# Kernel tuning notes

Hardware: AMD Instinct MI355X
Metric: run time of the kernel (lower is better)

The kernel has to match this reference:

```python
import jax, jax.numpy as jnp
import numpy as np

N_NODES = 50000
N_EDGES = 400000
D = 300          # num_features == hidden_units
L = 5            # num_layers
C = 128          # num_outputs
NG = 256         # graphs per batch
BN_EPS = 1e-5


def setup_inputs() -> dict:
    key = jax.random.key(0)
    ks = jax.random.split(key, 16)
    x = jax.random.normal(ks[0], (N_NODES, D), dtype=jnp.float32)
    edge_index = jax.random.randint(ks[1], (2, N_EDGES), 0, N_NODES, dtype=jnp.int64)
    batch = jnp.sort(jax.random.randint(ks[2], (N_NODES,), 0, NG, dtype=jnp.int64))
    s = 1.0 / np.sqrt(D)
    # Stacked per-layer GINConv MLP params: Linear -> BN -> ReLU -> Linear, then outer BN
    mlp_W1 = jax.random.uniform(ks[3], (L, D, D), jnp.float32, -s, s)
    mlp_b1 = jax.random.uniform(ks[4], (L, D), jnp.float32, -s, s)
    mlp_g1 = jnp.ones((L, D), jnp.float32)
    mlp_be1 = jnp.zeros((L, D), jnp.float32)
    mlp_W2 = jax.random.uniform(ks[5], (L, D, D), jnp.float32, -s, s)
    mlp_b2 = jax.random.uniform(ks[6], (L, D), jnp.float32, -s, s)
    bn_g = jnp.ones((L, D), jnp.float32)
    bn_b = jnp.zeros((L, D), jnp.float32)
    # num_layers+1 readout heads (num_features == hidden_units so all [D, C])
    fc_W = jax.random.uniform(ks[7], (L + 1, D, C), jnp.float32, -s, s)
    fc_b = jax.random.uniform(ks[8], (L + 1, C), jnp.float32, -s, s)
    return dict(x=x, edge_index=edge_index, batch=batch,
                mlp_W1=mlp_W1, mlp_b1=mlp_b1, mlp_g1=mlp_g1, mlp_be1=mlp_be1,
                mlp_W2=mlp_W2, mlp_b2=mlp_b2, bn_g=bn_g, bn_b=bn_b,
                fc_W=fc_W, fc_b=fc_b)


def _bn(h, gamma, beta):
    # BatchNorm1d in training mode: biased batch stats over the node dim
    mu = h.mean(axis=0)
    var = h.var(axis=0)
    return (h - mu) * jax.lax.rsqrt(var + BN_EPS) * gamma + beta


def reference(x, edge_index, batch, mlp_W1, mlp_b1, mlp_g1, mlp_be1,
              mlp_W2, mlp_b2, bn_g, bn_b, fc_W, fc_b):
    src, dst = edge_index[0], edge_index[1]
    n = x.shape[0]
    outs = [x]
    h = x
    for i in range(L):
        # GINConv (eps=0): MLP(x + sum_{j in N(i)} x_j), scatter-add over edges
        agg = jax.ops.segment_sum(h[src], dst, num_segments=n)
        z = h + agg
        z = z @ mlp_W1[i] + mlp_b1[i]
        z = jax.nn.relu(_bn(z, mlp_g1[i], mlp_be1[i]))
        z = z @ mlp_W2[i] + mlp_b2[i]
        h = jax.nn.relu(_bn(z, bn_g[i], bn_b[i]))  # outer BN + ReLU
        outs.append(h)
    # global mean pool per graph, then per-depth linear heads summed (dropout off in eval)
    counts = jax.ops.segment_sum(jnp.ones((n,), x.dtype), batch, num_segments=NG)
    inv = 1.0 / jnp.maximum(counts, 1.0)
    out = jnp.zeros((NG, C), x.dtype)
    for i, hi in enumerate(outs):
        pooled = jax.ops.segment_sum(hi, batch, num_segments=NG) * inv[:, None]
        out = out + (pooled @ fc_W[i] + fc_b[i])
    return out
```

## Files before the change

kernel.cpp:

```cpp
#include <hip/hip_runtime.h>

#define D 300
#define KP 320
#define NPAD 50048
#define NT128 391
#define NTPAD 392
#define PSL 3136
#define PSLIVE 3128
#define WSTRIDE 328
#define NGR 256
#define NL 5
#define NC 128
#define BN_EPS 1e-5f

typedef __attribute__((ext_vector_type(8))) short bf16x8;
typedef __attribute__((ext_vector_type(4))) float f32x4;
typedef unsigned short u16;

__device__ __forceinline__ void atomAdd(float* p, float v) { unsafeAtomicAdd(p, v); }

__device__ __forceinline__ short f2bf(float f) {
    union { float f; unsigned u; } v; v.f = f;
    unsigned r = v.u + 0x7fffu + ((v.u >> 16) & 1u);
    return (short)(r >> 16);
}
__device__ __forceinline__ float bf2f(short s) {
    union { unsigned u; float f; } v;
    v.u = ((unsigned)(u16)s) << 16;
    return v.f;
}
__device__ __forceinline__ unsigned cvtpk(float lo, float hi) {
    unsigned r;
    asm("v_cvt_pk_bf16_f32 %0, %1, %2" : "=v"(r) : "v"(lo), "v"(hi));
    return r;
}
template<int C>
__device__ __forceinline__ float rs_add(float v) {
    int x = __builtin_amdgcn_update_dpp(0, __float_as_int(v), C, 0xF, 0xF, true);
    return v + __int_as_float(x);
}
__device__ __forceinline__ float red16(float v) {
    v = rs_add<0x111>(v);
    v = rs_add<0x112>(v);
    v = rs_add<0x114>(v);
    v = rs_add<0x118>(v);
    return v;
}

__global__ void offsets_kernel(const int* __restrict__ batch, int* __restrict__ off, int N) {
    int g = threadIdx.x;
    if (g > NGR) return;
    int lo = 0, hi = N;
    while (lo < hi) {
        int mid = (lo + hi) >> 1;
        if (batch[mid] < g) lo = mid + 1; else hi = mid;
    }
    off[g] = lo;
}

__global__ __launch_bounds__(256)
void deg_kernel(const int* __restrict__ ei, int* __restrict__ deg, int E) {
    int e = blockIdx.x * 256 + threadIdx.x;
    if (e < E) atomicAdd(&deg[ei[E + e]], 1);
}

__global__ __launch_bounds__(256)
void degpart_kernel(const int* __restrict__ deg, int* __restrict__ part, int N) {
    int i = blockIdx.x * 256 + threadIdx.x;
    int v = (i < N) ? deg[i] : 0;
    #pragma unroll
    for (int o = 1; o < 64; o <<= 1) v += __shfl_xor(v, o);
    __shared__ int ws[4];
    if ((threadIdx.x & 63) == 0) ws[threadIdx.x >> 6] = v;
    __syncthreads();
    if (threadIdx.x == 0) part[blockIdx.x] = ws[0] + ws[1] + ws[2] + ws[3];
}

__global__ __launch_bounds__(256)
void partscan_kernel(int* __restrict__ part, int nb) {
    __shared__ int buf[256];
    int t = threadIdx.x;
    int v = (t < nb) ? part[t] : 0;
    buf[t] = v;
    __syncthreads();
    for (int o = 1; o < 256; o <<= 1) {
        int u = (t >= o) ? buf[t - o] : 0;
        __syncthreads();
        buf[t] += u;
        __syncthreads();
    }
    if (t < nb) part[t] = (t == 0) ? 0 : buf[t - 1];
}

__global__ __launch_bounds__(256)
void rowptr_kernel(const int* __restrict__ deg, const int* __restrict__ part,
                   int* __restrict__ rowptr, int N, int E) {
    __shared__ int buf[256];
    int b = blockIdx.x, t = threadIdx.x;
    int i = b * 256 + t;
    int v = (i < N) ? deg[i] : 0;
    buf[t] = v;
    __syncthreads();
    for (int o = 1; o < 256; o <<= 1) {
        int u = (t >= o) ? buf[t - o] : 0;
        __syncthreads();
        buf[t] += u;
        __syncthreads();
    }
    if (i < N) rowptr[i] = part[b] + buf[t] - v;
    if (b == 0 && t == 0) rowptr[N] = E;
}

__global__ __launch_bounds__(256)
void fill_kernel(const int* __restrict__ ei, const int* __restrict__ rowptr,
                 int* __restrict__ cursor, int* __restrict__ col, int E) {
    int e = blockIdx.x * 256 + threadIdx.x;
    if (e >= E) return;
    int src = ei[e];
    int dst = ei[E + e];
    int pos = atomicAdd(&cursor[dst], 1);
    col[rowptr[dst] + pos] = src;
}

__global__ __launch_bounds__(256)
void wcvt_kernel(const float* __restrict__ W1, const float* __restrict__ W2,
                 u16* __restrict__ Wt) {
    int idx = blockIdx.x * 256 + threadIdx.x;
    if (idx >= 10 * KP * 80) return;
    int n4 = idx % 80;
    int k = (idx / 80) % KP;
    int mat = idx / (80 * KP);
    const float* Wsrc = (mat < NL) ? (W1 + (size_t)mat * D * D) : (W2 + (size_t)(mat - NL) * D * D);
    float4 w = make_float4(0.f, 0.f, 0.f, 0.f);
    if (k < D && n4 < 75) w = *(const float4*)(Wsrc + (size_t)k * D + n4 * 4);
    size_t base = ((size_t)mat * 320 + n4 * 4) * KP + k;
    Wt[base]          = (u16)f2bf(w.x);
    Wt[base + KP]     = (u16)f2bf(w.y);
    Wt[base + 2 * KP] = (u16)f2bf(w.z);
    Wt[base + 3 * KP] = (u16)f2bf(w.w);
}

__global__ __launch_bounds__(256)
void xcvt_kernel(const float* __restrict__ x, u16* __restrict__ xbf, int N) {
    int idx = blockIdx.x * 256 + threadIdx.x;
    if (idx >= NPAD * 40) return;
    int row = idx / 40;
    int c8 = (idx - row * 40) * 8;
    short o[8];
    #pragma unroll
    for (int i = 0; i < 8; ++i) {
        int c = c8 + i;
        float f = (row < N && c < D) ? x[(size_t)row * D + c] : 0.f;
        o[i] = f2bf(f);
    }
    *(bf16x8*)(xbf + (size_t)row * KP + c8) = *(bf16x8*)o;
}

template<bool APPLY>
__global__ __launch_bounds__(256)
void gather_kernel(const u16* __restrict__ H, u16* __restrict__ Z,
                   const int* __restrict__ rowptr, const int* __restrict__ col,
                   const float* __restrict__ scsh, int N) {
    int idx = blockIdx.x * 256 + threadIdx.x;
    if (idx >= N * 40) return;
    int node = idx / 40;
    int c8 = (idx - node * 40) * 8;
    float sc[8], sh[8];
    if (APPLY) {
        #pragma unroll
        for (int i = 0; i < 8; ++i) { sc[i] = scsh[c8 + i]; sh[i] = scsh[KP + c8 + i]; }
    }
    int s = rowptr[node], e = rowptr[node + 1];
    bf16x8 v = *(const bf16x8*)(H + (size_t)node * KP + c8);
    float acc[8];
    #pragma unroll
    for (int i = 0; i < 8; ++i) {
        float f = bf2f(v[i]);
        acc[i] = APPLY ? fmaxf(fmaf(f, sc[i], sh[i]), 0.f) : f;
    }
    int j = s;
    for (; j + 4 <= e; j += 4) {
        int s0 = col[j], s1 = col[j + 1], s2 = col[j + 2], s3 = col[j + 3];
        bf16x8 w0 = *(const bf16x8*)(H + (size_t)s0 * KP + c8);
        bf16x8 w1 = *(const bf16x8*)(H + (size_t)s1 * KP + c8);
        bf16x8 w2 = *(const bf16x8*)(H + (size_t)s2 * KP + c8);
        bf16x8 w3 = *(const bf16x8*)(H + (size_t)s3 * KP + c8);
        #pragma unroll
        for (int i = 0; i < 8; ++i) {
            float f0 = bf2f(w0[i]);
            float f1 = bf2f(w1[i]);
            float f2 = bf2f(w2[i]);
            float f3 = bf2f(w3[i]);
            acc[i] += APPLY ? fmaxf(fmaf(f0, sc[i], sh[i]), 0.f) : f0;
            acc[i] += APPLY ? fmaxf(fmaf(f1, sc[i], sh[i]), 0.f) : f1;
            acc[i] += APPLY ? fmaxf(fmaf(f2, sc[i], sh[i]), 0.f) : f2;
            acc[i] += APPLY ? fmaxf(fmaf(f3, sc[i], sh[i]), 0.f) : f3;
        }
    }
    for (; j < e; ++j) {
        int s0 = col[j];
        bf16x8 w0 = *(const bf16x8*)(H + (size_t)s0 * KP + c8);
        #pragma unroll
        for (int i = 0; i < 8; ++i) {
            float f0 = bf2f(w0[i]);
            acc[i] += APPLY ? fmaxf(fmaf(f0, sc[i], sh[i]), 0.f) : f0;
        }
    }
    short o[8];
    #pragma unroll
    for (int i = 0; i < 8; ++i) o[i] = f2bf(acc[i]);
    *(bf16x8*)(Z + (size_t)node * KP + c8) = *(bf16x8*)o;
}

template<bool APPLY>
__global__ __launch_bounds__(320)
void pool_kernel(const u16* __restrict__ H, const int* __restrict__ off,
                 const float* __restrict__ scsh, float* __restrict__ pooled_l) {
    __shared__ float red[8][KP];
    int t = threadIdx.x;
    int g = blockIdx.x;
    int rq = t / 40;
    int c8 = (t - rq * 40) * 8;
    float sc[8], sh[8];
    if (APPLY) {
        #pragma unroll
        for (int i = 0; i < 8; ++i) { sc[i] = scsh[c8 + i]; sh[i] = scsh[KP + c8 + i]; }
    }
    int r0 = off[g], r1 = off[g + 1];
    float a[8] = {};
    for (int r = r0 + rq; r < r1; r += 8) {
        bf16x8 v = *(const bf16x8*)(H + (size_t)r * KP + c8);
        #pragma unroll
        for (int i = 0; i < 8; ++i) {
            float f = bf2f(v[i]);
            a[i] += APPLY ? fmaxf(fmaf(f, sc[i], sh[i]), 0.f) : f;
        }
    }
    #pragma unroll
    for (int i = 0; i < 8; ++i) red[rq][c8 + i] = a[i];
    __syncthreads();
    int c = t;
    if (c < D) {
        float s = 0.f;
        #pragma unroll
        for (int j = 0; j < 8; ++j) s += red[j][c];
        pooled_l[g * D + c] = s;
    }
}

template<bool APPLY>
__global__ __launch_bounds__(512, 6)
void mfma_gemm_kernel(const u16* __restrict__ Abf, const u16* __restrict__ Wt,
                      const float* __restrict__ scsh,
                      u16* __restrict__ Cbf, float* __restrict__ psum, int Nreal) {
    __shared__ u16 Ws[80 * WSTRIDE];
    const int tid = threadIdx.x;
    const int bid = blockIdx.x;
    const int xcd = bid & 7;
    const int pos = bid >> 3;
    const int tile = xcd + ((pos >> 2) << 3);
    const int nBase = (pos & 3) * 80;
    if (tile >= NT128) return;
    const int wave = tid >> 6, lane = tid & 63;
    const int quad = lane >> 4, l16 = lane & 15;

    const u16* pA = Abf + (size_t)(tile * 128 + wave * 16 + l16) * KP + quad * 8;
    bf16x8 a[10];
    #pragma unroll
    for (int kc = 0; kc < 10; ++kc) a[kc] = *(const bf16x8*)(pA + kc * 32);

    {
        const u16* src = Wt + (size_t)nBase * KP;
        for (int unit = tid; unit < 80 * 40; unit += 512) {
            int n = unit / 40, kg = unit - n * 40;
            int kc = kg >> 2, q = kg & 3;
            *(bf16x8*)&Ws[n * WSTRIDE + kc * 32 + ((q ^ (n & 3)) << 3)] =
                *(const bf16x8*)(src + (size_t)n * KP + kg * 8);
        }
    }

    #pragma unroll
    for (int kc = 0; kc < 10; ++kc) asm volatile("" : "+v"(a[kc]));
    __syncthreads();

    if (APPLY) {
        #pragma unroll
        for (int kc = 0; kc < 10; ++kc) {
            const float* sp = scsh + kc * 32 + quad * 8;
            float4 s0 = *(const float4*)sp;
            float4 s1 = *(const float4*)(sp + 4);
            float4 h0 = *(const float4*)(sp + KP);
            float4 h1 = *(const float4*)(sp + KP + 4);
            float sc[8] = {s0.x, s0.y, s0.z, s0.w, s1.x, s1.y, s1.z, s1.w};
            float sh[8] = {h0.x, h0.y, h0.z, h0.w, h1.x, h1.y, h1.z, h1.w};
            float f[8];
            #pragma unroll
            for (int i = 0; i < 8; ++i)
                f[i] = fmaxf(fmaf(bf2f(a[kc][i]), sc[i], sh[i]), 0.f);
            union { unsigned u[4]; bf16x8 v; } o;
            o.u[0] = cvtpk(f[0], f[1]);
            o.u[1] = cvtpk(f[2], f[3]);
            o.u[2] = cvtpk(f[4], f[5]);
            o.u[3] = cvtpk(f[6], f[7]);
            a[kc] = o.v;
        }
    }

    int wb[5];
    #pragma unroll
    for (int nt = 0; nt < 5; ++nt)
        wb[nt] = (nt * 16 + l16) * WSTRIDE + ((quad ^ (l16 & 3)) << 3);

    f32x4 acc[5] = {};
    __builtin_amdgcn_s_setprio(1);
    #pragma unroll
    for (int kc = 0; kc < 10; ++kc) {
        #pragma unroll
        for (int nt = 0; nt < 5; ++nt) {
            bf16x8 b = *(const bf16x8*)&Ws[wb[nt] + kc * 32];
            acc[nt] = __builtin_amdgcn_mfma_f32_16x16x32_bf16(b, a[kc], acc[nt], 0, 0, 0);
        }
    }
    __builtin_amdgcn_s_setprio(0);

    const int r0g = tile * 128 + wave * 16 + l16;
    const bool ok = r0g < Nreal;
    u16* crow = Cbf + (size_t)r0g * KP + nBase + quad * 4;
    const int pslot = tile * 8 + wave;
    float* psq = psum + (size_t)320 * PSL;
    #pragma unroll
    for (int nt = 0; nt < 5; ++nt) {
        float v0 = acc[nt][0], v1 = acc[nt][1], v2 = acc[nt][2], v3 = acc[nt][3];
        uint2 w;
        w.x = cvtpk(v0, v1);
        w.y = cvtpk(v2, v3);
        *(uint2*)(crow + nt * 16) = w;
        float m0 = ok ? v0 : 0.f, m1 = ok ? v1 : 0.f;
        float m2 = ok ? v2 : 0.f, m3 = ok ? v3 : 0.f;
        float sv0 = red16(m0), qv0 = red16(m0 * m0);
        float sv1 = red16(m1), qv1 = red16(m1 * m1);
        float sv2 = red16(m2), qv2 = red16(m2 * m2);
        float sv3 = red16(m3), qv3 = red16(m3 * m3);
        if (l16 == 15) {
            int c = nBase + nt * 16 + quad * 4;
            psum[(size_t)(c + 0) * PSL + pslot] = sv0;
            psum[(size_t)(c + 1) * PSL + pslot] = sv1;
            psum[(size_t)(c + 2) * PSL + pslot] = sv2;
            psum[(size_t)(c + 3) * PSL + pslot] = sv3;
            psq [(size_t)(c + 0) * PSL + pslot] = qv0;
            psq [(size_t)(c + 1) * PSL + pslot] = qv1;
            psq [(size_t)(c + 2) * PSL + pslot] = qv2;
            psq [(size_t)(c + 3) * PSL + pslot] = qv3;
        }
    }
}

__global__ __launch_bounds__(256)
void bnfin_kernel(const float* __restrict__ psum, const float* __restrict__ g,
                  const float* __restrict__ be, float* __restrict__ scsh, float invN) {
    int c = blockIdx.x;
    const float* ps = psum + (size_t)c * PSL;
    const float* pq = psum + (size_t)(320 + c) * PSL;
    float s1 = 0.f, s2 = 0.f;
    for (int i = threadIdx.x; i < PSLIVE; i += 256) { s1 += ps[i]; s2 += pq[i]; }
    #pragma unroll
    for (int o = 1; o < 64; o <<= 1) { s1 += __shfl_xor(s1, o); s2 += __shfl_xor(s2, o); }
    __shared__ float w1[4], w2[4];
    int wv = threadIdx.x >> 6;
    if ((threadIdx.x & 63) == 0) { w1[wv] = s1; w2[wv] = s2; }
    __syncthreads();
    if (threadIdx.x == 0) {
        float t1 = w1[0] + w1[1] + w1[2] + w1[3];
        float t2 = w2[0] + w2[1] + w2[2] + w2[3];
        float mu = t1 * invN;
        float var = t2 * invN - mu * mu;
        float s = g[c] / sqrtf(var + BN_EPS);
        scsh[c] = s;
        scsh[KP + c] = fmaf(-mu, s, be[c]);
    }
}

__global__ __launch_bounds__(128)
void bias_init_kernel(const float* __restrict__ fcb, float* __restrict__ out) {
    int i = blockIdx.x * 128 + threadIdx.x;
    if (i >= NGR * NC) return;
    int c = i & (NC - 1);
    float s = 0.f;
    for (int l = 0; l <= NL; ++l) s += fcb[l * NC + c];
    out[i] = s;
}

__global__ __launch_bounds__(128)
void readout_kernel(const float* __restrict__ pooled, const int* __restrict__ off,
                    const float* __restrict__ fcW, float* __restrict__ out) {
    __shared__ float sp[4][D];
    int c = threadIdx.x;
    int l = blockIdx.y;
    int g0 = blockIdx.x * 4;
    for (int i = c; i < 4 * D; i += 128) {
        int gg = i / D, k = i - gg * D;
        sp[gg][k] = pooled[((size_t)l * NGR + g0 + gg) * D + k];
    }
    __syncthreads();
    float acc[4] = {0.f, 0.f, 0.f, 0.f};
    for (int k = 0; k < D; ++k) {
        float w = fcW[((size_t)l * D + k) * NC + c];
        #pragma unroll
        for (int gg = 0; gg < 4; ++gg) acc[gg] = fmaf(sp[gg][k], w, acc[gg]);
    }
    #pragma unroll
    for (int gg = 0; gg < 4; ++gg) {
        int g = g0 + gg;
        float inv = 1.0f / fmaxf((float)(off[g + 1] - off[g]), 1.0f);
        atomAdd(&out[g * NC + c], acc[gg] * inv);
    }
}

extern "C" void kernel_launch(void* const* d_in, const int* in_sizes, int n_in,
                              void* d_out, int out_size, void* d_ws, size_t ws_size,
                              hipStream_t stream) {
    const float* x       = (const float*)d_in[0];
    const int*   ei      = (const int*)d_in[1];
    const int*   batch   = (const int*)d_in[2];
    const float* W1  = (const float*)d_in[3];
    const float* g1  = (const float*)d_in[5];
    const float* be1 = (const float*)d_in[6];
    const float* W2  = (const float*)d_in[7];
    const float* bng = (const float*)d_in[9];
    const float* bnb = (const float*)d_in[10];
    const float* fcW = (const float*)d_in[11];
    const float* fcb = (const float*)d_in[12];
    float* out = (float*)d_out;

    const int N = in_sizes[0] / D;
    const int E = in_sizes[1] / 2;
    const int nb = (N + 255) / 256;

    u16* xbf  = (u16*)d_ws;
    float* psum = (float*)d_ws;
    u16* bufA = xbf + (size_t)NPAD * KP;
    u16* bufB = bufA + (size_t)NPAD * KP;
    u16* Wt   = bufB + (size_t)NPAD * KP;
    float* pooled = (float*)(Wt + (size_t)10 * 320 * KP);
    float* sc1    = pooled + (size_t)(NL + 1) * NGR * D;
    float* sc2    = sc1 + 2 * KP;
    int*   off    = (int*)(sc2 + 2 * KP);
    int*   rowptr = off + NGR + 1;
    int*   cursor = rowptr + N + 1;
    int*   col    = cursor + N;
    int*   part   = col + E;

    hipMemsetAsync(sc1, 0, 4 * KP * sizeof(float), stream);
    offsets_kernel<<<1, 320, 0, stream>>>(batch, off, N);
    bias_init_kernel<<<(NGR * NC + 127) / 128, 128, 0, stream>>>(fcb, out);

    hipMemsetAsync(cursor, 0, N * sizeof(int), stream);
    deg_kernel<<<(E + 255) / 256, 256, 0, stream>>>(ei, cursor, E);
    degpart_kernel<<<nb, 256, 0, stream>>>(cursor, part, N);
    partscan_kernel<<<1, 256, 0, stream>>>(part, nb);
    rowptr_kernel<<<nb, 256, 0, stream>>>(cursor, part, rowptr, N, E);
    hipMemsetAsync(cursor, 0, N * sizeof(int), stream);
    fill_kernel<<<(E + 255) / 256, 256, 0, stream>>>(ei, rowptr, cursor, col, E);

    wcvt_kernel<<<(10 * KP * 80 + 255) / 256, 256, 0, stream>>>(W1, W2, Wt);
    xcvt_kernel<<<(NPAD * 40 + 255) / 256, 256, 0, stream>>>(x, xbf, N);

    const int gemm_blocks = 8 * 49 * 4;
    const int nd40 = N * 40;
    float invN = 1.0f / (float)N;
    const size_t WtM = (size_t)320 * KP;

    pool_kernel<false><<<NGR, 320, 0, stream>>>(xbf, off, sc2, pooled);

    u16* g = bufA;
    u16* t = bufB;
    const u16* src = xbf;
    for (int l = 0; l < NL; ++l) {
        if (l == 0)
            gather_kernel<false><<<(nd40 + 255) / 256, 256, 0, stream>>>(src, g, rowptr, col, sc2, N);
        else
            gather_kernel<true><<<(nd40 + 255) / 256, 256, 0, stream>>>(src, g, rowptr, col, sc2, N);
        mfma_gemm_kernel<false><<<gemm_blocks, 512, 0, stream>>>(
            g, Wt + (size_t)l * WtM, sc1, t, psum, N);
        bnfin_kernel<<<D, 256, 0, stream>>>(psum, g1 + l * D, be1 + l * D, sc1, invN);
        mfma_gemm_kernel<true><<<gemm_blocks, 512, 0, stream>>>(
            t, Wt + (size_t)(NL + l) * WtM, sc1, g, psum, N);
        bnfin_kernel<<<D, 256, 0, stream>>>(psum, bng + l * D, bnb + l * D, sc2, invN);
        pool_kernel<true><<<NGR, 320, 0, stream>>>(g, off, sc2, pooled + (size_t)(l + 1) * NGR * D);
        src = g;
        u16* tmp = g; g = t; t = tmp;
    }
    readout_kernel<<<dim3(NGR / 4, NL + 1), 128, 0, stream>>>(pooled, off, fcW, out);
}
```

Measured before the change: 1.058 ms.

## Swap GEMM operand roles: weights in registers, activation tile via direct LDS loads

The MFMA GEMM now keeps each wave's 16-column slice of the weight matrix in registers and stages the 128-row activation tile into LDS using global_load_lds direct copies. Each of 5 waves covers all 8 row groups, and the fused BN+ReLU apply runs in place on the LDS tile. Per-tile BN partial sums are accumulated across row groups before the cross-lane reduction, which shrinks the partial-sum buffer from per-wave to per-tile slots. The block grows to 80KB of LDS with 320 threads and a lower occupancy hint. This trades occupancy for fewer redundant weight loads and less reduction work.

```diff
diff --git a/kernel.cpp b/kernel.cpp
--- a/kernel.cpp
+++ b/kernel.cpp
@@ -4,10 +4,8 @@
 #define KP 320
 #define NPAD 50048
 #define NT128 391
-#define NTPAD 392
-#define PSL 3136
-#define PSLIVE 3128
-#define WSTRIDE 328
+#define PSL 392
+#define PSLIVE 391
 #define NGR 256
 #define NL 5
 #define NC 128
@@ -45,6 +43,10 @@
     v = rs_add<0x114>(v);
     v = rs_add<0x118>(v);
     return v;
+}
+__device__ __forceinline__ void gload_lds16(const u16* g, u16* l) {
+    __builtin_amdgcn_global_load_lds((const __attribute__((address_space(1))) void*)g,
+                                     (__attribute__((address_space(3))) void*)l, 16, 0, 0);
 }
 
 __global__ void offsets_kernel(const int* __restrict__ batch, int* __restrict__ off, int N) {
@@ -249,11 +251,11 @@
 }
 
 template<bool APPLY>
-__global__ __launch_bounds__(512, 6)
+__global__ __launch_bounds__(320, 2)
 void mfma_gemm_kernel(const u16* __restrict__ Abf, const u16* __restrict__ Wt,
                       const float* __restrict__ scsh,
                       u16* __restrict__ Cbf, float* __restrict__ psum, int Nreal) {
-    __shared__ u16 Ws[80 * WSTRIDE];
+    __shared__ u16 Ab[40960];
     const int tid = threadIdx.x;
     const int bid = blockIdx.x;
     const int xcd = bid & 7;
@@ -261,96 +263,102 @@
     const int tile = xcd + ((pos >> 2) << 3);
     const int nBase = (pos & 3) * 80;
     if (tile >= NT128) return;
-    const int wave = tid >> 6, lane = tid & 63;
+    const int wave = tid >> 6;
+    const int lane = tid & 63;
     const int quad = lane >> 4, l16 = lane & 15;
 
-    const u16* pA = Abf + (size_t)(tile * 128 + wave * 16 + l16) * KP + quad * 8;
-    bf16x8 a[10];
-    #pragma unroll
-    for (int kc = 0; kc < 10; ++kc) a[kc] = *(const bf16x8*)(pA + kc * 32);
-
+    bf16x8 bw[10];
     {
-        const u16* src = Wt + (size_t)nBase * KP;
-        for (int unit = tid; unit < 80 * 40; unit += 512) {
-            int n = unit / 40, kg = unit - n * 40;
-            int kc = kg >> 2, q = kg & 3;
-            *(bf16x8*)&Ws[n * WSTRIDE + kc * 32 + ((q ^ (n & 3)) << 3)] =
-                *(const bf16x8*)(src + (size_t)n * KP + kg * 8);
-        }
-    }
-
-    #pragma unroll
-    for (int kc = 0; kc < 10; ++kc) asm volatile("" : "+v"(a[kc]));
+        const u16* wp = Wt + (size_t)(nBase + wave * 16 + l16) * KP + quad * 8;
+        #pragma unroll
+        for (int kc = 0; kc < 10; ++kc) bw[kc] = *(const bf16x8*)(wp + kc * 32);
+    }
+
+    {
+        const u16* base = Abf + (size_t)tile * 128 * KP;
+        #pragma unroll
+        for (int i = 0; i < 16; ++i) {
+            int c = i * 320 + tid;
+            int t6 = c >> 6;
+            int rg = (t6 * 205) >> 11;
+            int kc = t6 - rg * 10;
+            int go = (rg * 16 + l16) * KP + kc * 32 + quad * 8;
+            gload_lds16(base + go, &Ab[c * 8]);
+        }
+    }
     __syncthreads();
 
     if (APPLY) {
-        #pragma unroll
-        for (int kc = 0; kc < 10; ++kc) {
-            const float* sp = scsh + kc * 32 + quad * 8;
-            float4 s0 = *(const float4*)sp;
-            float4 s1 = *(const float4*)(sp + 4);
-            float4 h0 = *(const float4*)(sp + KP);
-            float4 h1 = *(const float4*)(sp + KP + 4);
-            float sc[8] = {s0.x, s0.y, s0.z, s0.w, s1.x, s1.y, s1.z, s1.w};
-            float sh[8] = {h0.x, h0.y, h0.z, h0.w, h1.x, h1.y, h1.z, h1.w};
+        float sca[2][8], sha[2][8];
+        #pragma unroll
+        for (int h = 0; h < 2; ++h) {
+            int k0 = (2 * wave + h) * 32 + quad * 8;
+            float4 s0 = *(const float4*)(scsh + k0);
+            float4 s1 = *(const float4*)(scsh + k0 + 4);
+            float4 h0 = *(const float4*)(scsh + KP + k0);
+            float4 h1 = *(const float4*)(scsh + KP + k0 + 4);
+            sca[h][0]=s0.x; sca[h][1]=s0.y; sca[h][2]=s0.z; sca[h][3]=s0.w;
+            sca[h][4]=s1.x; sca[h][5]=s1.y; sca[h][6]=s1.z; sca[h][7]=s1.w;
+            sha[h][0]=h0.x; sha[h][1]=h0.y; sha[h][2]=h0.z; sha[h][3]=h0.w;
+            sha[h][4]=h1.x; sha[h][5]=h1.y; sha[h][6]=h1.z; sha[h][7]=h1.w;
+        }
+        #pragma unroll
+        for (int j = 0; j < 16; ++j) {
+            const int h = j & 1, rg = j >> 1;
+            u16* p = &Ab[((rg * 10 + 2 * wave + h) << 9) + lane * 8];
+            bf16x8 v = *(const bf16x8*)p;
             float f[8];
             #pragma unroll
             for (int i = 0; i < 8; ++i)
-                f[i] = fmaxf(fmaf(bf2f(a[kc][i]), sc[i], sh[i]), 0.f);
+                f[i] = fmaxf(fmaf(bf2f(v[i]), sca[h][i], sha[h][i]), 0.f);
             union { unsigned u[4]; bf16x8 v; } o;
             o.u[0] = cvtpk(f[0], f[1]);
             o.u[1] = cvtpk(f[2], f[3]);
             o.u[2] = cvtpk(f[4], f[5]);
             o.u[3] = cvtpk(f[6], f[7]);
-            a[kc] = o.v;
-        }
-    }
-
-    int wb[5];
-    #pragma unroll
-    for (int nt = 0; nt < 5; ++nt)
-        wb[nt] = (nt * 16 + l16) * WSTRIDE + ((quad ^ (l16 & 3)) << 3);
-
-    f32x4 acc[5] = {};
+            *(bf16x8*)p = o.v;
+        }
+        __syncthreads();
+    }
+
+    const int lbase = lane * 8;
+    f32x4 acc[8] = {};
     __builtin_amdgcn_s_setprio(1);
     #pragma unroll
     for (int kc = 0; kc < 10; ++kc) {
         #pragma unroll
-        for (int nt = 0; nt < 5; ++nt) {
-            bf16x8 b = *(const bf16x8*)&Ws[wb[nt] + kc * 32];
-            acc[nt] = __builtin_amdgcn_mfma_f32_16x16x32_bf16(b, a[kc], acc[nt], 0, 0, 0);
+        for (int rg = 0; rg < 8; ++rg) {
+            bf16x8 af = *(const bf16x8*)&Ab[(((rg * 10 + kc)) << 9) + lbase];
+            acc[rg] = __builtin_amdgcn_mfma_f32_16x16x32_bf16(bw[kc], af, acc[rg], 0, 0, 0);
         }
     }
     __builtin_amdgcn_s_setprio(0);
 
-    const int r0g = tile * 128 + wave * 16 + l16;
-    const bool ok = r0g < Nreal;
-    u16* crow = Cbf + (size_t)r0g * KP + nBase + quad * 4;
-    const int pslot = tile * 8 + wave;
-    float* psq = psum + (size_t)320 * PSL;
-    #pragma unroll
-    for (int nt = 0; nt < 5; ++nt) {
-        float v0 = acc[nt][0], v1 = acc[nt][1], v2 = acc[nt][2], v3 = acc[nt][3];
+    const int c0 = nBase + wave * 16 + quad * 4;
+    u16* crow = Cbf + (size_t)(tile * 128 + l16) * KP + c0;
+    float s[4] = {0.f, 0.f, 0.f, 0.f}, q[4] = {0.f, 0.f, 0.f, 0.f};
+    #pragma unroll
+    for (int rg = 0; rg < 8; ++rg) {
+        const int row = tile * 128 + rg * 16 + l16;
+        const bool ok = row < Nreal;
+        float v0 = acc[rg][0], v1 = acc[rg][1], v2 = acc[rg][2], v3 = acc[rg][3];
         uint2 w;
         w.x = cvtpk(v0, v1);
         w.y = cvtpk(v2, v3);
-        *(uint2*)(crow + nt * 16) = w;
+        *(uint2*)(crow + (size_t)(rg * 16) * KP) = w;
         float m0 = ok ? v0 : 0.f, m1 = ok ? v1 : 0.f;
         float m2 = ok ? v2 : 0.f, m3 = ok ? v3 : 0.f;
-        float sv0 = red16(m0), qv0 = red16(m0 * m0);
-        float sv1 = red16(m1), qv1 = red16(m1 * m1);
-        float sv2 = red16(m2), qv2 = red16(m2 * m2);
-        float sv3 = red16(m3), qv3 = red16(m3 * m3);
+        s[0] += m0; s[1] += m1; s[2] += m2; s[3] += m3;
+        q[0] = fmaf(m0, m0, q[0]); q[1] = fmaf(m1, m1, q[1]);
+        q[2] = fmaf(m2, m2, q[2]); q[3] = fmaf(m3, m3, q[3]);
+    }
+    #pragma unroll
+    for (int r = 0; r < 4; ++r) {
+        float sv = red16(s[r]);
+        float qv = red16(q[r]);
         if (l16 == 15) {
-            int c = nBase + nt * 16 + quad * 4;
-            psum[(size_t)(c + 0) * PSL + pslot] = sv0;
-            psum[(size_t)(c + 1) * PSL + pslot] = sv1;
-            psum[(size_t)(c + 2) * PSL + pslot] = sv2;
-            psum[(size_t)(c + 3) * PSL + pslot] = sv3;
-            psq [(size_t)(c + 0) * PSL + pslot] = qv0;
-            psq [(size_t)(c + 1) * PSL + pslot] = qv1;
-            psq [(size_t)(c + 2) * PSL + pslot] = qv2;
-            psq [(size_t)(c + 3) * PSL + pslot] = qv3;
+            psum[(size_t)(c0 + r) * PSL + tile] = sv;
+            psum[(size_t)(320 + c0 + r) * PSL + tile] = qv;
         }
     }
 }
@@ -480,10 +488,10 @@
             gather_kernel<false><<<(nd40 + 255) / 256, 256, 0, stream>>>(src, g, rowptr, col, sc2, N);
         else
             gather_kernel<true><<<(nd40 + 255) / 256, 256, 0, stream>>>(src, g, rowptr, col, sc2, N);
-        mfma_gemm_kernel<false><<<gemm_blocks, 512, 0, stream>>>(
+        mfma_gemm_kernel<false><<<gemm_blocks, 320, 0, stream>>>(
             g, Wt + (size_t)l * WtM, sc1, t, psum, N);
         bnfin_kernel<<<D, 256, 0, stream>>>(psum, g1 + l * D, be1 + l * D, sc1, invN);
-        mfma_gemm_kernel<true><<<gemm_blocks, 512, 0, stream>>>(
+        mfma_gemm_kernel<true><<<gemm_blocks, 320, 0, stream>>>(
             t, Wt + (size_t)(NL + l) * WtM, sc1, g, psum, N);
         bnfin_kernel<<<D, 256, 0, stream>>>(psum, bng + l * D, bnb + l * D, sc2, invN);
         pool_kernel<true><<<NGR, 320, 0, stream>>>(g, off, sc2, pooled + (size_t)(l + 1) * NGR * D);
```

New measurement: 1.093 ms. 3.3% more time.
